# Kernel optimization log

Measured on AMD Instinct MI355X. Metric: run time of the kernel, lower is better.

The kernel has to match this reference:

```python
import jax, jax.numpy as jnp
import numpy as np

N = 100000
E = 1600000
IN_DIM = 128
HID = 64
EPS = 1e-5


def setup_inputs() -> dict:
    key = jax.random.key(0)
    ks = jax.random.split(key, 16)
    inp = {
        "x": jax.random.normal(ks[0], (N, IN_DIM), dtype=jnp.float32),
        "edge_index": jax.random.randint(ks[1], (2, E), 0, N, dtype=jnp.int64),
    }
    dims = [(HID, IN_DIM), (HID, HID), (HID, HID)]
    for i, (o, c) in enumerate(dims):
        inp[f"W{i}"] = jax.random.normal(ks[2 + 4 * i], (o, c), dtype=jnp.float32) / np.sqrt(c)
        inp[f"b{i}"] = jnp.zeros((o,), dtype=jnp.float32)
        inp[f"g{i}"] = jnp.ones((o,), dtype=jnp.float32)
        inp[f"be{i}"] = jnp.zeros((o,), dtype=jnp.float32)
    return inp


def _gcn_layer(x, W, b, src, dst, norm):
    # PyG GCNConv: linear first, then normalized sum aggregation, then bias
    h = x @ W.T                                  # [N, out]
    msg = h[src] * norm[:, None]                 # [E+N, out] gather (memory-bound)
    agg = jax.ops.segment_sum(msg, dst, num_segments=N)
    return agg + b


def _batchnorm(h, g, be):
    mean = jnp.mean(h, axis=0)
    var = jnp.mean((h - mean) ** 2, axis=0)      # biased var (training-mode BN)
    return (h - mean) * jax.lax.rsqrt(var + EPS) * g + be


def reference(x, edge_index, W0, b0, g0, be0, W1, b1, g1, be1, W2, b2, g2, be2):
    # add self loops (GCNConv default)
    loops = jnp.arange(N, dtype=edge_index.dtype)
    src = jnp.concatenate([edge_index[0], loops])
    dst = jnp.concatenate([edge_index[1], loops])
    # symmetric normalization: deg^{-1/2}[src] * deg^{-1/2}[dst]
    deg = jax.ops.segment_sum(jnp.ones_like(dst, dtype=x.dtype), dst, num_segments=N)
    dis = jax.lax.rsqrt(jnp.maximum(deg, 1.0))
    norm = dis[src] * dis[dst]

    params = [(W0, b0, g0, be0), (W1, b1, g1, be1), (W2, b2, g2, be2)]
    for W, b, g, be in params:
        h = _gcn_layer(x, W, b, src, dst, norm)
        h = _batchnorm(h, g, be)
        h = jax.nn.relu(h)
        x = x + h if h.shape == x.shape else h   # residual from layer 2 on
    return x
```

## Files before the change

### kernel.cpp

```cpp
#include <hip/hip_runtime.h>
#include <math.h>

#define NN 100000
#define NE 1600000
#define EPS_BN 1e-5f
#define NB 1000
#define BSZ 100
#define PCHUNK 8192

__device__ __forceinline__ unsigned bf16r(float x) {
  unsigned u = __float_as_uint(x);
  return (u + 0x7FFFu + ((u >> 16) & 1u)) >> 16;
}
__device__ __forceinline__ float bf16lo(unsigned w) { return __uint_as_float(w << 16); }
__device__ __forceinline__ float bf16hi(unsigned w) { return __uint_as_float(w & 0xFFFF0000u); }

__global__ void detect_kernel(const int* __restrict__ ei32, int* __restrict__ flag) {
  __shared__ int red[256];
  int t = threadIdx.x;
  int acc = 0;
#pragma unroll
  for (int k = 0; k < 4; ++k) acc |= ei32[2 * (t * 4 + k) + 1];
  red[t] = acc;
  __syncthreads();
  for (int off = 128; off > 0; off >>= 1) {
    if (t < off) red[t] |= red[t + off];
    __syncthreads();
  }
  if (t == 0) *flag = (red[0] == 0) ? 1 : 0;
}

__device__ __forceinline__ int edge_at(const void* ei, long long idx, int is64) {
  if (is64) return (int)((const long long*)ei)[idx];
  return ((const int*)ei)[idx];
}

__global__ __launch_bounds__(256) void bhist_kernel(const void* __restrict__ ei,
                                                    const int* __restrict__ flag,
                                                    int* __restrict__ bucket_cnt) {
  __shared__ int h[NB];
  int is64 = *flag;
  int t = threadIdx.x;
  for (int k = t; k < NB; k += 256) h[k] = 0;
  __syncthreads();
  for (int e = blockIdx.x * 256 + t; e < NE; e += gridDim.x * 256) {
    int d = edge_at(ei, (long long)NE + e, is64);
    atomicAdd(&h[d / BSZ], 1);
  }
  __syncthreads();
  for (int k = t; k < NB; k += 256) {
    int v = h[k];
    if (v) atomicAdd(&bucket_cnt[k], v);
  }
}

__global__ __launch_bounds__(1024) void bscan_kernel(const int* __restrict__ bucket_cnt,
                                                     int* __restrict__ bucket_base,
                                                     int* __restrict__ bucket_put,
                                                     int* __restrict__ row_start) {
  __shared__ int sh[1024];
  int t = threadIdx.x;
  int v = (t < NB) ? bucket_cnt[t] : 0;
  sh[t] = v;
  __syncthreads();
  for (int off = 1; off < 1024; off <<= 1) {
    int u = (t >= off) ? sh[t - off] : 0;
    __syncthreads();
    sh[t] += u;
    __syncthreads();
  }
  if (t < NB) {
    int b = sh[t] - v;
    bucket_base[t] = b;
    bucket_put[t] = b;
  }
  if (t == 0) row_start[NN] = NE;
}

__global__ __launch_bounds__(256) void bplace_kernel(const void* __restrict__ ei,
                                                     const int* __restrict__ flag,
                                                     int* __restrict__ bucket_put,
                                                     unsigned* __restrict__ staging) {
  __shared__ int hist[NB];
  __shared__ int base[NB];
  int is64 = *flag;
  int t = threadIdx.x;
  long long e0 = (long long)blockIdx.x * PCHUNK;
  int n = (int)min((long long)PCHUNK, (long long)NE - e0);
  for (int k = t; k < NB; k += 256) hist[k] = 0;
  __syncthreads();
  for (int k = t; k < n; k += 256) {
    int d = edge_at(ei, (long long)NE + e0 + k, is64);
    atomicAdd(&hist[d / BSZ], 1);
  }
  __syncthreads();
  for (int k = t; k < NB; k += 256) {
    int c = hist[k];
    base[k] = c ? atomicAdd(&bucket_put[k], c) : 0;
    hist[k] = 0;
  }
  __syncthreads();
  for (int k = t; k < n; k += 256) {
    int s = edge_at(ei, e0 + k, is64);
    int d = edge_at(ei, (long long)NE + e0 + k, is64);
    int b = d / BSZ;
    int p = base[b] + atomicAdd(&hist[b], 1);
    staging[p] = ((unsigned)s << 7) | (unsigned)(d - b * BSZ);
  }
}

__global__ __launch_bounds__(256) void bbuild_kernel(const unsigned* __restrict__ staging,
                                                     const int* __restrict__ bucket_base,
                                                     const int* __restrict__ bucket_cnt,
                                                     int* __restrict__ row_start,
                                                     float* __restrict__ dis,
                                                     int* __restrict__ csr_src) {
  __shared__ int deg[BSZ];
  __shared__ int excl[128];
  __shared__ int cur[BSZ];
  int b = blockIdx.x;
  int t = threadIdx.x;
  int base = bucket_base[b], cnt = bucket_cnt[b];
  for (int k = t; k < BSZ; k += 256) {
    deg[k] = 0;
    cur[k] = 0;
  }
  __syncthreads();
  for (int e = t; e < cnt; e += 256) {
    unsigned w = staging[base + e];
    atomicAdd(&deg[w & 127], 1);
  }
  __syncthreads();
  if (t < 128) excl[t] = (t < BSZ) ? deg[t] : 0;
  __syncthreads();
  for (int off = 1; off < 128; off <<= 1) {
    int u = 0;
    if (t < 128 && t >= off) u = excl[t - off];
    __syncthreads();
    if (t < 128) excl[t] += u;
    __syncthreads();
  }
  if (t < BSZ) {
    int ex = excl[t] - deg[t];
    row_start[b * BSZ + t] = base + ex;
    dis[b * BSZ + t] = rsqrtf((float)(deg[t] + 1));
    excl[t] = ex;
  }
  __syncthreads();
  for (int e = t; e < cnt; e += 256) {
    unsigned w = staging[base + e];
    int dl = w & 127;
    int p = base + excl[dl] + atomicAdd(&cur[dl], 1);
    csr_src[p] = (int)(w >> 7);
  }
}

template <int K>
__global__ __launch_bounds__(256) void gemm_kernel(const float* __restrict__ x,
                                                   const float* __restrict__ Wm,
                                                   const float* __restrict__ dis,
                                                   unsigned* __restrict__ h16) {
  constexpr int KC = K / 4;
  __shared__ float4 ws4[64 * KC];
  __shared__ float4 xs4[64 * KC];
  int t = threadIdx.x;
  int row0 = blockIdx.x * 64;
  const float4* W4 = (const float4*)Wm;
  for (int idx = t; idx < 64 * KC; idx += 256) {
    int j = idx / KC, kc = idx % KC;
    ws4[j * KC + (kc ^ (j & 7))] = W4[idx];
  }
  const float4* x4 = (const float4*)x;
  for (int idx = t; idx < 64 * KC; idx += 256) {
    int r = idx / KC, kc = idx % KC;
    int row = row0 + r;
    float4 v = make_float4(0.f, 0.f, 0.f, 0.f);
    if (row < NN) v = x4[(size_t)row * KC + kc];
    xs4[r * KC + kc] = v;
  }
  __syncthreads();
  int j = t & 63, wv = t >> 6;
  float acc[16];
#pragma unroll
  for (int r = 0; r < 16; ++r) acc[r] = 0.f;
  for (int kc = 0; kc < KC; ++kc) {
    float4 w = ws4[j * KC + (kc ^ (j & 7))];
#pragma unroll
    for (int r = 0; r < 16; ++r) {
      float4 xv = xs4[(wv * 16 + r) * KC + kc];
      acc[r] += w.x * xv.x + w.y * xv.y + w.z * xv.z + w.w * xv.w;
    }
  }
#pragma unroll
  for (int r = 0; r < 16; ++r) {
    int row = row0 + wv * 16 + r;
    float di = (row < NN) ? dis[row] : 0.f;
    float a = acc[r] * di;
    float part = __shfl_xor(a, 1, 64);
    if (row < NN && !(j & 1)) {
      h16[(size_t)row * 32 + (j >> 1)] = bf16r(a) | (bf16r(part) << 16);
    }
  }
}

__global__ __launch_bounds__(256) void agg_kernel(const unsigned* __restrict__ h16,
                                                  const int* __restrict__ row_start,
                                                  const int* __restrict__ csr_src,
                                                  const float* __restrict__ dis,
                                                  float4* __restrict__ agg4,
                                                  float* __restrict__ stats) {
  const uint2* h2 = (const uint2*)h16;
  int t = threadIdx.x, lane = t & 63, wv = t >> 6;
  int c = lane & 15;
  int g = lane >> 4;
  int gw = blockIdx.x * 4 + wv;
  int nw = gridDim.x * 4;
  float s0 = 0.f, s1 = 0.f, s2 = 0.f, s3 = 0.f;
  float q0 = 0.f, q1 = 0.f, q2 = 0.f, q3 = 0.f;
  for (int i0 = gw; i0 < NN; i0 += nw) {
    int i = __builtin_amdgcn_readfirstlane(i0);
    int beg = row_start[i], end = row_start[i + 1];
    float di = dis[i];
    uint2 ws = h2[(size_t)i * 16 + c];
    float sw = (g == 0) ? 1.f : 0.f;
    float a0 = bf16lo(ws.x) * sw, a1 = bf16hi(ws.x) * sw;
    float a2 = bf16lo(ws.y) * sw, a3 = bf16hi(ws.y) * sw;
    int e = beg;
    for (; e + 8 <= end; e += 8) {
      int r0 = csr_src[e], r1 = csr_src[e + 1], r2 = csr_src[e + 2], r3 = csr_src[e + 3];
      int r4 = csr_src[e + 4], r5 = csr_src[e + 5], r6 = csr_src[e + 6], r7 = csr_src[e + 7];
      int ra = (g == 0) ? r0 : (g == 1) ? r1 : (g == 2) ? r2 : r3;
      int rb = (g == 0) ? r4 : (g == 1) ? r5 : (g == 2) ? r6 : r7;
      uint2 wa = h2[(size_t)ra * 16 + c];
      uint2 wb = h2[(size_t)rb * 16 + c];
      a0 += bf16lo(wa.x);
      a1 += bf16hi(wa.x);
      a2 += bf16lo(wa.y);
      a3 += bf16hi(wa.y);
      a0 += bf16lo(wb.x);
      a1 += bf16hi(wb.x);
      a2 += bf16lo(wb.y);
      a3 += bf16hi(wb.y);
    }
    if (e + 4 <= end) {
      int r0 = csr_src[e], r1 = csr_src[e + 1], r2 = csr_src[e + 2], r3 = csr_src[e + 3];
      int ra = (g == 0) ? r0 : (g == 1) ? r1 : (g == 2) ? r2 : r3;
      uint2 wa = h2[(size_t)ra * 16 + c];
      a0 += bf16lo(wa.x);
      a1 += bf16hi(wa.x);
      a2 += bf16lo(wa.y);
      a3 += bf16hi(wa.y);
      e += 4;
    }
    if (e < end) {
      int last = end - 1;
      int r0 = csr_src[e];
      int r1 = csr_src[min(e + 1, last)];
      int r2 = csr_src[min(e + 2, last)];
      int r3 = csr_src[min(e + 3, last)];
      int ra = (g == 0) ? r0 : (g == 1) ? r1 : (g == 2) ? r2 : r3;
      float wt = (e + g < end) ? 1.f : 0.f;
      uint2 wa = h2[(size_t)ra * 16 + c];
      a0 += bf16lo(wa.x) * wt;
      a1 += bf16hi(wa.x) * wt;
      a2 += bf16lo(wa.y) * wt;
      a3 += bf16hi(wa.y) * wt;
    }
#pragma unroll
    for (int m = 16; m <= 32; m <<= 1) {
      a0 += __shfl_xor(a0, m, 64);
      a1 += __shfl_xor(a1, m, 64);
      a2 += __shfl_xor(a2, m, 64);
      a3 += __shfl_xor(a3, m, 64);
    }
    a0 *= di;
    a1 *= di;
    a2 *= di;
    a3 *= di;
    if (lane < 16) {
      agg4[(size_t)i * 16 + c] = make_float4(a0, a1, a2, a3);
      s0 += a0;
      s1 += a1;
      s2 += a2;
      s3 += a3;
      q0 += a0 * a0;
      q1 += a1 * a1;
      q2 += a2 * a2;
      q3 += a3 * a3;
    }
  }
  __shared__ float redS[4][64];
  __shared__ float redQ[4][64];
  if (lane < 16) {
    redS[wv][4 * c + 0] = s0;
    redS[wv][4 * c + 1] = s1;
    redS[wv][4 * c + 2] = s2;
    redS[wv][4 * c + 3] = s3;
    redQ[wv][4 * c + 0] = q0;
    redQ[wv][4 * c + 1] = q1;
    redQ[wv][4 * c + 2] = q2;
    redQ[wv][4 * c + 3] = q3;
  }
  __syncthreads();
  if (wv == 0) {
    float a = redS[0][lane] + redS[1][lane] + redS[2][lane] + redS[3][lane];
    float b = redQ[0][lane] + redQ[1][lane] + redQ[2][lane] + redQ[3][lane];
    atomicAdd(&stats[lane], a);
    atomicAdd(&stats[64 + lane], b);
  }
}

__global__ void bnp_kernel(const float* __restrict__ stats, const float* __restrict__ g,
                           const float* __restrict__ be, float* __restrict__ bnp) {
  int f = threadIdx.x;
  if (f < 64) {
    float m = stats[f] / (float)NN;
    float v = stats[64 + f] / (float)NN - m * m;
    float sc = g[f] * rsqrtf(fmaxf(v, 0.f) + EPS_BN);
    bnp[f] = sc;
    bnp[64 + f] = be[f] - m * sc;
  }
}

template <bool RES>
__global__ __launch_bounds__(256) void apply_kernel(const float* __restrict__ agg,
                                                    const float* __restrict__ bnp,
                                                    const float* __restrict__ xres,
                                                    float* __restrict__ out) {
  __shared__ float sc[64], sh[64];
  int t = threadIdx.x;
  if (t < 64) {
    sc[t] = bnp[t];
    sh[t] = bnp[64 + t];
  }
  __syncthreads();
  const int total4 = NN * 16;
  for (int i = blockIdx.x * blockDim.x + t; i < total4; i += gridDim.x * blockDim.x) {
    float4 a = ((const float4*)agg)[i];
    int f = (i * 4) & 63;
    float4 y;
    y.x = fmaxf(fmaf(a.x, sc[f], sh[f]), 0.f);
    y.y = fmaxf(fmaf(a.y, sc[f + 1], sh[f + 1]), 0.f);
    y.z = fmaxf(fmaf(a.z, sc[f + 2], sh[f + 2]), 0.f);
    y.w = fmaxf(fmaf(a.w, sc[f + 3], sh[f + 3]), 0.f);
    if (RES) {
      float4 xr = ((const float4*)xres)[i];
      y.x += xr.x;
      y.y += xr.y;
      y.z += xr.z;
      y.w += xr.w;
    }
    ((float4*)out)[i] = y;
  }
}

extern "C" void kernel_launch(void* const* d_in, const int* in_sizes, int n_in,
                              void* d_out, int out_size, void* d_ws, size_t ws_size,
                              hipStream_t stream) {
  const float* x0 = (const float*)d_in[0];
  const void* ei = d_in[1];
  const float* W0 = (const float*)d_in[2];
  const float* g0 = (const float*)d_in[4];
  const float* be0 = (const float*)d_in[5];
  const float* W1 = (const float*)d_in[6];
  const float* g1 = (const float*)d_in[8];
  const float* be1 = (const float*)d_in[9];
  const float* W2 = (const float*)d_in[10];
  const float* g2 = (const float*)d_in[12];
  const float* be2 = (const float*)d_in[13];
  float* out = (float*)d_out;

  char* p = (char*)d_ws;
  auto carve = [&](size_t bytes) {
    char* q = p;
    p += (bytes + 255) & ~(size_t)255;
    return (void*)q;
  };
  float* bufA = (float*)carve((size_t)NN * 64 * 4);
  unsigned* h16 = (unsigned*)carve((size_t)NN * 32 * 4);
  float* bufC = (float*)carve((size_t)NN * 64 * 4);
  int* row_start = (int*)carve((size_t)(NN + 1) * 4);
  float* dis = (float*)carve((size_t)NN * 4);
  int* csr_src = (int*)carve((size_t)NE * 4);
  unsigned* staging = (unsigned*)carve((size_t)NE * 4);
  int* bucket_cnt = (int*)carve(NB * 4);
  int* bucket_base = (int*)carve(NB * 4);
  int* bucket_put = (int*)carve(NB * 4);
  float* stats = (float*)carve(128 * 4);
  float* bnp = (float*)carve(128 * 4);
  int* flag = (int*)carve(256);

  detect_kernel<<<1, 256, 0, stream>>>((const int*)ei, flag);
  hipMemsetAsync(bucket_cnt, 0, NB * 4, stream);
  bhist_kernel<<<256, 256, 0, stream>>>(ei, flag, bucket_cnt);
  bscan_kernel<<<1, 1024, 0, stream>>>(bucket_cnt, bucket_base, bucket_put, row_start);
  const int place_blocks = (NE + PCHUNK - 1) / PCHUNK;
  bplace_kernel<<<place_blocks, 256, 0, stream>>>(ei, flag, bucket_put, staging);
  bbuild_kernel<<<NB, 256, 0, stream>>>(staging, bucket_base, bucket_cnt, row_start, dis,
                                        csr_src);

  const int gemm_blocks = (NN + 63) / 64;

  hipMemsetAsync(stats, 0, 128 * 4, stream);
  gemm_kernel<128><<<gemm_blocks, 256, 0, stream>>>(x0, W0, dis, h16);
  agg_kernel<<<2048, 256, 0, stream>>>(h16, row_start, csr_src, dis, (float4*)bufC, stats);
  bnp_kernel<<<1, 64, 0, stream>>>(stats, g0, be0, bnp);
  apply_kernel<false><<<1024, 256, 0, stream>>>(bufC, bnp, nullptr, bufA);

  hipMemsetAsync(stats, 0, 128 * 4, stream);
  gemm_kernel<64><<<gemm_blocks, 256, 0, stream>>>(bufA, W1, dis, h16);
  agg_kernel<<<2048, 256, 0, stream>>>(h16, row_start, csr_src, dis, (float4*)bufC, stats);
  bnp_kernel<<<1, 64, 0, stream>>>(stats, g1, be1, bnp);
  apply_kernel<true><<<1024, 256, 0, stream>>>(bufC, bnp, bufA, out);

  hipMemsetAsync(stats, 0, 128 * 4, stream);
  gemm_kernel<64><<<gemm_blocks, 256, 0, stream>>>(out, W2, dis, h16);
  agg_kernel<<<2048, 256, 0, stream>>>(h16, row_start, csr_src, dis, (float4*)bufC, stats);
  bnp_kernel<<<1, 64, 0, stream>>>(stats, g2, be2, bnp);
  apply_kernel<true><<<1024, 256, 0, stream>>>(bufC, bnp, out, out);
}
```

Baseline: 470.0 us.

## Fuse BN-apply/ReLU/residual into next layer's GEMM load and drop bnp kernels

The batchnorm parameter computation moves into a per-block prologue, and the BN+ReLU+residual apply step is folded into the next layer's GEMM input-staging loop. That loop writes the activated rows to global memory while also placing them in shared memory. This removes two standalone apply passes, three bnp launches and a re-read of the activations by the GEMM. Each layer gets its own stats buffer, so all three are zeroed with one memset up front. The cost is that every GEMM block recomputes the 64 BN scale and shift values from stats.

```diff
diff --git a/kernel.cpp b/kernel.cpp
--- a/kernel.cpp
+++ b/kernel.cpp
@@ -155,6 +155,19 @@
   }
 }
 
+__device__ __forceinline__ void bn_prologue(const float* __restrict__ stats,
+                                            const float* __restrict__ g,
+                                            const float* __restrict__ be, float* scb,
+                                            float* shb, int t) {
+  if (t < 64) {
+    float m = stats[t] / (float)NN;
+    float v = stats[64 + t] / (float)NN - m * m;
+    float sc = g[t] * rsqrtf(fmaxf(v, 0.f) + EPS_BN);
+    scb[t] = sc;
+    shb[t] = be[t] - m * sc;
+  }
+}
+
 template <int K>
 __global__ __launch_bounds__(256) void gemm_kernel(const float* __restrict__ x,
                                                    const float* __restrict__ Wm,
@@ -177,6 +190,73 @@
     float4 v = make_float4(0.f, 0.f, 0.f, 0.f);
     if (row < NN) v = x4[(size_t)row * KC + kc];
     xs4[r * KC + kc] = v;
+  }
+  __syncthreads();
+  int j = t & 63, wv = t >> 6;
+  float acc[16];
+#pragma unroll
+  for (int r = 0; r < 16; ++r) acc[r] = 0.f;
+  for (int kc = 0; kc < KC; ++kc) {
+    float4 w = ws4[j * KC + (kc ^ (j & 7))];
+#pragma unroll
+    for (int r = 0; r < 16; ++r) {
+      float4 xv = xs4[(wv * 16 + r) * KC + kc];
+      acc[r] += w.x * xv.x + w.y * xv.y + w.z * xv.z + w.w * xv.w;
+    }
+  }
+#pragma unroll
+  for (int r = 0; r < 16; ++r) {
+    int row = row0 + wv * 16 + r;
+    float di = (row < NN) ? dis[row] : 0.f;
+    float a = acc[r] * di;
+    float part = __shfl_xor(a, 1, 64);
+    if (row < NN && !(j & 1)) {
+      h16[(size_t)row * 32 + (j >> 1)] = bf16r(a) | (bf16r(part) << 16);
+    }
+  }
+}
+
+template <bool RES>
+__global__ __launch_bounds__(256) void gemmF_kernel(
+    const float4* __restrict__ aggp, const float* __restrict__ stats,
+    const float* __restrict__ g, const float* __restrict__ be,
+    const float4* __restrict__ xres, float4* __restrict__ xout,
+    const float* __restrict__ Wm, const float* __restrict__ dis,
+    unsigned* __restrict__ h16) {
+  constexpr int KC = 16;
+  __shared__ float4 ws4[64 * KC];
+  __shared__ float4 xs4[64 * KC];
+  __shared__ float scb[64], shb[64];
+  int t = threadIdx.x;
+  int row0 = blockIdx.x * 64;
+  bn_prologue(stats, g, be, scb, shb, t);
+  const float4* W4 = (const float4*)Wm;
+  for (int idx = t; idx < 64 * KC; idx += 256) {
+    int j = idx / KC, kc = idx % KC;
+    ws4[j * KC + (kc ^ (j & 7))] = W4[idx];
+  }
+  __syncthreads();
+  for (int idx = t; idx < 64 * KC; idx += 256) {
+    int r = idx / KC, kc = idx % KC;
+    int row = row0 + r;
+    float4 y = make_float4(0.f, 0.f, 0.f, 0.f);
+    if (row < NN) {
+      float4 a = aggp[(size_t)row * KC + kc];
+      int f = kc * 4;
+      y.x = fmaxf(fmaf(a.x, scb[f], shb[f]), 0.f);
+      y.y = fmaxf(fmaf(a.y, scb[f + 1], shb[f + 1]), 0.f);
+      y.z = fmaxf(fmaf(a.z, scb[f + 2], shb[f + 2]), 0.f);
+      y.w = fmaxf(fmaf(a.w, scb[f + 3], shb[f + 3]), 0.f);
+      if (RES) {
+        float4 xr = xres[(size_t)row * KC + kc];
+        y.x += xr.x;
+        y.y += xr.y;
+        y.z += xr.z;
+        y.w += xr.w;
+      }
+      xout[(size_t)row * KC + kc] = y;
+    }
+    xs4[r * KC + kc] = y;
   }
   __syncthreads();
   int j = t & 63, wv = t >> 6;
@@ -310,46 +390,30 @@
   }
 }
 
-__global__ void bnp_kernel(const float* __restrict__ stats, const float* __restrict__ g,
-                           const float* __restrict__ be, float* __restrict__ bnp) {
-  int f = threadIdx.x;
-  if (f < 64) {
-    float m = stats[f] / (float)NN;
-    float v = stats[64 + f] / (float)NN - m * m;
-    float sc = g[f] * rsqrtf(fmaxf(v, 0.f) + EPS_BN);
-    bnp[f] = sc;
-    bnp[64 + f] = be[f] - m * sc;
-  }
-}
-
-template <bool RES>
-__global__ __launch_bounds__(256) void apply_kernel(const float* __restrict__ agg,
-                                                    const float* __restrict__ bnp,
-                                                    const float* __restrict__ xres,
-                                                    float* __restrict__ out) {
-  __shared__ float sc[64], sh[64];
-  int t = threadIdx.x;
-  if (t < 64) {
-    sc[t] = bnp[t];
-    sh[t] = bnp[64 + t];
-  }
+__global__ __launch_bounds__(256) void applyF_kernel(const float* __restrict__ agg,
+                                                     const float* __restrict__ stats,
+                                                     const float* __restrict__ g,
+                                                     const float* __restrict__ be,
+                                                     const float* __restrict__ xres,
+                                                     float* __restrict__ out) {
+  __shared__ float scb[64], shb[64];
+  int t = threadIdx.x;
+  bn_prologue(stats, g, be, scb, shb, t);
   __syncthreads();
   const int total4 = NN * 16;
   for (int i = blockIdx.x * blockDim.x + t; i < total4; i += gridDim.x * blockDim.x) {
     float4 a = ((const float4*)agg)[i];
     int f = (i * 4) & 63;
     float4 y;
-    y.x = fmaxf(fmaf(a.x, sc[f], sh[f]), 0.f);
-    y.y = fmaxf(fmaf(a.y, sc[f + 1], sh[f + 1]), 0.f);
-    y.z = fmaxf(fmaf(a.z, sc[f + 2], sh[f + 2]), 0.f);
-    y.w = fmaxf(fmaf(a.w, sc[f + 3], sh[f + 3]), 0.f);
-    if (RES) {
-      float4 xr = ((const float4*)xres)[i];
-      y.x += xr.x;
-      y.y += xr.y;
-      y.z += xr.z;
-      y.w += xr.w;
-    }
+    y.x = fmaxf(fmaf(a.x, scb[f], shb[f]), 0.f);
+    y.y = fmaxf(fmaf(a.y, scb[f + 1], shb[f + 1]), 0.f);
+    y.z = fmaxf(fmaf(a.z, scb[f + 2], shb[f + 2]), 0.f);
+    y.w = fmaxf(fmaf(a.w, scb[f + 3], shb[f + 3]), 0.f);
+    float4 xr = ((const float4*)xres)[i];
+    y.x += xr.x;
+    y.y += xr.y;
+    y.z += xr.z;
+    y.w += xr.w;
     ((float4*)out)[i] = y;
   }
 }
@@ -386,12 +450,14 @@
   int* bucket_cnt = (int*)carve(NB * 4);
   int* bucket_base = (int*)carve(NB * 4);
   int* bucket_put = (int*)carve(NB * 4);
-  float* stats = (float*)carve(128 * 4);
-  float* bnp = (float*)carve(128 * 4);
+  float* stats0 = (float*)carve(128 * 4);
+  float* stats1 = (float*)carve(128 * 4);
+  float* stats2 = (float*)carve(128 * 4);
   int* flag = (int*)carve(256);
 
   detect_kernel<<<1, 256, 0, stream>>>((const int*)ei, flag);
   hipMemsetAsync(bucket_cnt, 0, NB * 4, stream);
+  hipMemsetAsync(stats0, 0, 3 * 128 * 4, stream);
   bhist_kernel<<<256, 256, 0, stream>>>(ei, flag, bucket_cnt);
   bscan_kernel<<<1, 1024, 0, stream>>>(bucket_cnt, bucket_base, bucket_put, row_start);
   const int place_blocks = (NE + PCHUNK - 1) / PCHUNK;
@@ -401,21 +467,20 @@
 
   const int gemm_blocks = (NN + 63) / 64;
 
-  hipMemsetAsync(stats, 0, 128 * 4, stream);
   gemm_kernel<128><<<gemm_blocks, 256, 0, stream>>>(x0, W0, dis, h16);
-  agg_kernel<<<2048, 256, 0, stream>>>(h16, row_start, csr_src, dis, (float4*)bufC, stats);
-  bnp_kernel<<<1, 64, 0, stream>>>(stats, g0, be0, bnp);
-  apply_kernel<false><<<1024, 256, 0, stream>>>(bufC, bnp, nullptr, bufA);
-
-  hipMemsetAsync(stats, 0, 128 * 4, stream);
-  gemm_kernel<64><<<gemm_blocks, 256, 0, stream>>>(bufA, W1, dis, h16);
-  agg_kernel<<<2048, 256, 0, stream>>>(h16, row_start, csr_src, dis, (float4*)bufC, stats);
-  bnp_kernel<<<1, 64, 0, stream>>>(stats, g1, be1, bnp);
-  apply_kernel<true><<<1024, 256, 0, stream>>>(bufC, bnp, bufA, out);
-
-  hipMemsetAsync(stats, 0, 128 * 4, stream);
-  gemm_kernel<64><<<gemm_blocks, 256, 0, stream>>>(out, W2, dis, h16);
-  agg_kernel<<<2048, 256, 0, stream>>>(h16, row_start, csr_src, dis, (float4*)bufC, stats);
-  bnp_kernel<<<1, 64, 0, stream>>>(stats, g2, be2, bnp);
-  apply_kernel<true><<<1024, 256, 0, stream>>>(bufC, bnp, out, out);
-}
+  agg_kernel<<<2048, 256, 0, stream>>>(h16, row_start, csr_src, dis, (float4*)bufC,
+                                       stats0);
+
+  gemmF_kernel<false><<<gemm_blocks, 256, 0, stream>>>(
+      (const float4*)bufC, stats0, g0, be0, nullptr, (float4*)bufA, W1, dis, h16);
+  agg_kernel<<<2048, 256, 0, stream>>>(h16, row_start, csr_src, dis, (float4*)bufC,
+                                       stats1);
+
+  gemmF_kernel<true><<<gemm_blocks, 256, 0, stream>>>(
+      (const float4*)bufC, stats1, g1, be1, (const float4*)bufA, (float4*)out, W2, dis,
+      h16);
+  agg_kernel<<<2048, 256, 0, stream>>>(h16, row_start, csr_src, dis, (float4*)bufC,
+                                       stats2);
+
+  applyF_kernel<<<1024, 256, 0, stream>>>(bufC, stats2, g2, be2, out, out);
+}
```

Measured after the change: 444.3 us. -5.5%, faster.
